# Performance work log

Hardware: AMD Instinct MI355X
Metric: run time of the kernel (lower is better)

The kernel has to match this reference:

```python
import jax, jax.numpy as jnp
import numpy as np
from jax import lax

BETA = 0.25  # args.beta

def setup_inputs() -> dict:
    key = jax.random.key(0)
    k1, k2 = jax.random.split(key)
    B, C, H, W = 32, 256, 32, 32
    K = 8192  # codebook_size; C == latent_dim
    z = jax.random.normal(k1, (B, C, H, W), dtype=jnp.float32)
    embedding = jax.random.normal(k2, (K, C), dtype=jnp.float32)
    return {"z": z, "embedding": embedding}

def reference(z, embedding):
    B, C, H, W = z.shape
    # rearrange 'b c h w -> b (h w) c'
    zf = z.reshape(B, C, H * W).transpose(0, 2, 1)  # [B, HW, C]
    # squared Euclidean distances (same argmin as torch.cdist): ||z||^2 - 2 z.e + ||e||^2
    d2 = (
        jnp.sum(zf * zf, axis=-1, keepdims=True)
        - 2.0 * jnp.einsum('bnc,kc->bnk', zf, embedding)
        + jnp.sum(embedding * embedding, axis=-1)
    )  # [B, HW, K]
    min_d = jnp.argmin(d2, axis=-1)  # [B, HW] int
    # faithful to original: .view((B, C, H, W)) is a raw reshape of [B, HW, C]
    z_q = embedding[min_d].reshape(B, C, H, W)
    commitment_loss = jnp.mean((lax.stop_gradient(z_q) - z) ** 2)
    codebook_loss = jnp.mean((lax.stop_gradient(z) - z_q) ** 2)
    loss = codebook_loss + BETA * commitment_loss
    # faithful to original straight-through variant: z - (z_q - z).detach()
    z_q_out = z - lax.stop_gradient(z_q - z)
    return z_q_out, min_d, loss
```

## Files before the change

kernel.cpp:

```cpp
#include <hip/hip_runtime.h>

#define CDIM    256
#define HWDIM   1024
#define KCB     8192
#define OUT_ZQ  8388608
#define OUT_MD  32768

__global__ void vq_init_kernel(float* p) {
    if (threadIdx.x == 0 && blockIdx.x == 0) p[0] = 0.0f;
}

__global__ __launch_bounds__(256) void vq_enorm_kernel(const float* __restrict__ emb,
                                                       float* __restrict__ enorm) {
    const int w    = threadIdx.x >> 6;
    const int lane = threadIdx.x & 63;
    const int k    = blockIdx.x * 4 + w;
    float4 v = *(const float4*)(emb + (size_t)k * CDIM + lane * 4);
    float s = v.x * v.x + v.y * v.y + v.z * v.z + v.w * v.w;
    #pragma unroll
    for (int off = 32; off > 0; off >>= 1) s += __shfl_down(s, off);
    if (lane == 0) enorm[k] = s;
}

__global__ __launch_bounds__(512) void vq_argmin_kernel(const float* __restrict__ z,
                                                        const float* __restrict__ emb,
                                                        const float* __restrict__ enorm,
                                                        float* __restrict__ mind_out) {
    __shared__ float zt[256][64];
    __shared__ float et[2][32][64];

    const int tid = threadIdx.x;
    const int tx  = tid & 15;
    const int ty  = tid >> 4;
    const int n0  = blockIdx.x * 64;
    const int b   = n0 >> 10;
    const int hw0 = n0 & 1023;
    const float* zb = z + (size_t)b * (CDIM * HWDIM) + hw0;

    for (int idx = tid; idx < 256 * 16; idx += 512) {
        const int c = idx >> 4, q4 = idx & 15;
        *(float4*)&zt[c][q4 * 4] = *(const float4*)(zb + (size_t)c * HWDIM + q4 * 4);
    }

    const int kk   = tid >> 3;
    const int c4   = tid & 7;
    const int ecol = kk ^ (c4 << 3);

    {
        float4 ev = *(const float4*)(emb + (size_t)kk * CDIM + c4 * 4);
        et[0][c4 * 4 + 0][ecol] = ev.x;
        et[0][c4 * 4 + 1][ecol] = ev.y;
        et[0][c4 * 4 + 2][ecol] = ev.z;
        et[0][c4 * 4 + 3][ecol] = ev.w;
    }
    __syncthreads();

    float bmin[2];
    int   bidx[2];
    #pragma unroll
    for (int i = 0; i < 2; ++i) { bmin[i] = 3.4e38f; bidx[i] = 0; }

    float acc[2][4];
    float4 en4;

    const int NCHUNK = (KCB / 64) * (CDIM / 32);
    int cur = 0;
    for (int t = 0; t < NCHUNK; ++t) {
        float4 nv;
        const bool hasnext = (t + 1) < NCHUNK;
        if (hasnext) {
            const int tn  = t + 1;
            const int nk0 = (tn >> 3) * 64;
            const int nc0 = (tn & 7) * 32;
            nv = *(const float4*)(emb + (size_t)(nk0 + kk) * CDIM + nc0 + c4 * 4);
        }
        if ((t & 7) == 0) {
            #pragma unroll
            for (int i = 0; i < 2; ++i)
                #pragma unroll
                for (int j = 0; j < 4; ++j) acc[i][j] = 0.0f;
            en4 = *(const float4*)(enorm + (t >> 3) * 64 + tx * 4);
        }
        const int c0 = (t & 7) * 32;

        #pragma unroll
        for (int ci = 0; ci < 32; ++ci) {
            float2 zf = *(const float2*)&zt[c0 + ci][ty * 2];
            float4 ef = *(const float4*)&et[cur][ci][(tx * 4) ^ ((ci >> 2) << 3)];
            const float* zp = reinterpret_cast<const float*>(&zf);
            const float* ep = reinterpret_cast<const float*>(&ef);
            #pragma unroll
            for (int i = 0; i < 2; ++i)
                #pragma unroll
                for (int j = 0; j < 4; ++j)
                    acc[i][j] += zp[i] * ep[j];
        }

        if (hasnext) {
            et[cur ^ 1][c4 * 4 + 0][ecol] = nv.x;
            et[cur ^ 1][c4 * 4 + 1][ecol] = nv.y;
            et[cur ^ 1][c4 * 4 + 2][ecol] = nv.z;
            et[cur ^ 1][c4 * 4 + 3][ecol] = nv.w;
        }

        if ((t & 7) == 7) {
            const int k0 = (t >> 3) * 64;
            const float* en = reinterpret_cast<const float*>(&en4);
            #pragma unroll
            for (int j = 0; j < 4; ++j) {
                const int kid = k0 + tx * 4 + j;
                #pragma unroll
                for (int i = 0; i < 2; ++i) {
                    const float s = en[j] - 2.0f * acc[i][j];
                    if (s < bmin[i]) { bmin[i] = s; bidx[i] = kid; }
                }
            }
        }
        __syncthreads();
        cur ^= 1;
    }

    float* redv = &zt[0][0];
    int*   redi = (int*)&zt[16][0];
    #pragma unroll
    for (int i = 0; i < 2; ++i) {
        const int q = ty * 2 + i;
        redv[q * 16 + tx] = bmin[i];
        redi[q * 16 + tx] = bidx[i];
    }
    __syncthreads();
    if (tid < 64) {
        const int q = tid;
        float bv = redv[q * 16 + 0];
        int   bi = redi[q * 16 + 0];
        #pragma unroll
        for (int t = 1; t < 16; ++t) {
            const float v = redv[q * 16 + t];
            const int  id = redi[q * 16 + t];
            if (v < bv || (v == bv && id < bi)) { bv = v; bi = id; }
        }
        mind_out[n0 + q] = (float)bi;
    }
}

__global__ __launch_bounds__(256) void vq_gather_kernel(const float* __restrict__ z,
                                                        const float* __restrict__ emb,
                                                        const float* __restrict__ mind,
                                                        float* __restrict__ out,
                                                        float* __restrict__ loss_accum) {
    const int tid = blockIdx.x * 256 + threadIdx.x;
    const int total4 = OUT_ZQ / 4;
    float lsum = 0.0f;
    for (int i4 = tid; i4 < total4; i4 += gridDim.x * 256) {
        const int idx = i4 * 4;
        const int b   = idx >> 18;
        const int f   = idx & 262143;
        const int nn  = f >> 8;
        const int cpr = f & 255;
        const int k   = (int)mind[b * 1024 + nn];
        float4 e4 = *(const float4*)(emb + (size_t)k * CDIM + cpr);
        float4 z4 = *(const float4*)(z + idx);
        float4 o;
        o.x = 2.0f * z4.x - e4.x;
        o.y = 2.0f * z4.y - e4.y;
        o.z = 2.0f * z4.z - e4.z;
        o.w = 2.0f * z4.w - e4.w;
        *(float4*)(out + idx) = o;
        const float dx = e4.x - z4.x, dy = e4.y - z4.y, dz = e4.z - z4.z, dw = e4.w - z4.w;
        lsum += dx * dx + dy * dy + dz * dz + dw * dw;
    }
    #pragma unroll
    for (int off = 32; off > 0; off >>= 1) lsum += __shfl_down(lsum, off);
    __shared__ float wsum[4];
    const int lane = threadIdx.x & 63, w = threadIdx.x >> 6;
    if (lane == 0) wsum[w] = lsum;
    __syncthreads();
    if (threadIdx.x == 0) atomicAdd(loss_accum, wsum[0] + wsum[1] + wsum[2] + wsum[3]);
}

__global__ void vq_final_kernel(float* lossp) {
    if (threadIdx.x == 0 && blockIdx.x == 0)
        lossp[0] = 1.25f * lossp[0] / 8388608.0f;
}

extern "C" void kernel_launch(void* const* d_in, const int* in_sizes, int n_in,
                              void* d_out, int out_size, void* d_ws, size_t ws_size,
                              hipStream_t stream) {
    const float* z   = (const float*)d_in[0];
    const float* emb = (const float*)d_in[1];
    float* out   = (float*)d_out;
    float* mind  = out + OUT_ZQ;
    float* lossp = out + OUT_ZQ + OUT_MD;
    float* enorm = out;

    vq_init_kernel<<<1, 64, 0, stream>>>(lossp);
    vq_enorm_kernel<<<2048, 256, 0, stream>>>(emb, enorm);
    vq_argmin_kernel<<<512, 512, 0, stream>>>(z, emb, enorm, mind);
    vq_gather_kernel<<<2048, 256, 0, stream>>>(z, emb, mind, out, lossp);
    vq_final_kernel<<<1, 64, 0, stream>>>(lossp);
}
```

Baseline: 2.358 ms.

## Compute distance GEMM with split-fp16 MFMA instead of scalar FP32 FMAs

The FP32 CUDA-core style distance tile loop is replaced by MFMA 16x16x32 fp16 instructions. Both z and the codebook are split into hi/lo fp16 parts so three products (hh, hl, lh) approximate the fp32 dot product. A new pre-kernel converts the codebook into swizzled hi/lo fp16 buffers held in scratch space in the output. The z operands stay resident in registers while codebook tiles are double-buffered through LDS, and the argmin reduction uses cross-lane shuffles. The split-fp16 scheme drops the lo*lo term and can lose accuracy, which risks changing argmin results on near-ties.

After: 1.915 ms. 18.8% less time.

```diff
diff --git a/kernel.cpp b/kernel.cpp
--- a/kernel.cpp
+++ b/kernel.cpp
@@ -5,6 +5,10 @@
 #define KCB     8192
 #define OUT_ZQ  8388608
 #define OUT_MD  32768
+#define KT      512
+
+typedef _Float16 f16x8 __attribute__((ext_vector_type(8)));
+typedef float    f32x4 __attribute__((ext_vector_type(4)));
 
 __global__ void vq_init_kernel(float* p) {
     if (threadIdx.x == 0 && blockIdx.x == 0) p[0] = 0.0f;
@@ -22,125 +26,163 @@
     if (lane == 0) enorm[k] = s;
 }
 
-__global__ __launch_bounds__(512) void vq_argmin_kernel(const float* __restrict__ z,
-                                                        const float* __restrict__ emb,
-                                                        const float* __restrict__ enorm,
-                                                        float* __restrict__ mind_out) {
-    __shared__ float zt[256][64];
-    __shared__ float et[2][32][64];
-
-    const int tid = threadIdx.x;
-    const int tx  = tid & 15;
-    const int ty  = tid >> 4;
-    const int n0  = blockIdx.x * 64;
-    const int b   = n0 >> 10;
-    const int hw0 = n0 & 1023;
-    const float* zb = z + (size_t)b * (CDIM * HWDIM) + hw0;
-
-    for (int idx = tid; idx < 256 * 16; idx += 512) {
-        const int c = idx >> 4, q4 = idx & 15;
-        *(float4*)&zt[c][q4 * 4] = *(const float4*)(zb + (size_t)c * HWDIM + q4 * 4);
-    }
-
-    const int kk   = tid >> 3;
-    const int c4   = tid & 7;
-    const int ecol = kk ^ (c4 << 3);
-
-    {
-        float4 ev = *(const float4*)(emb + (size_t)kk * CDIM + c4 * 4);
-        et[0][c4 * 4 + 0][ecol] = ev.x;
-        et[0][c4 * 4 + 1][ecol] = ev.y;
-        et[0][c4 * 4 + 2][ecol] = ev.z;
-        et[0][c4 * 4 + 3][ecol] = ev.w;
+__global__ __launch_bounds__(256) void vq_ecvt_kernel(const float* __restrict__ emb,
+                                                      _Float16* __restrict__ ehi,
+                                                      _Float16* __restrict__ elo) {
+    const int gid = blockIdx.x * 256 + threadIdx.x;
+    const int k = gid >> 5;
+    const int x = gid & 31;
+    const float* src = emb + (size_t)k * CDIM + x * 8;
+    float4 v0 = *(const float4*)(src);
+    float4 v1 = *(const float4*)(src + 4);
+    const float tmp[8] = {v0.x, v0.y, v0.z, v0.w, v1.x, v1.y, v1.z, v1.w};
+    f16x8 hi, lo;
+    #pragma unroll
+    for (int j = 0; j < 8; ++j) {
+        _Float16 h = (_Float16)tmp[j];
+        hi[j] = h;
+        lo[j] = (_Float16)(tmp[j] - (float)h);
+    }
+    const int xs = x ^ (k & 7);
+    *(f16x8*)(ehi + (size_t)k * CDIM + xs * 8) = hi;
+    *(f16x8*)(elo + (size_t)k * CDIM + xs * 8) = lo;
+}
+
+__global__ __launch_bounds__(128, 1) void vq_argmin_kernel(const float* __restrict__ z,
+                                                           const _Float16* __restrict__ ehi,
+                                                           const _Float16* __restrict__ elo,
+                                                           const float* __restrict__ enorm,
+                                                           float* __restrict__ mind_out) {
+    __shared__ _Float16 eb[2][2][16 * CDIM];
+
+    const int tid  = threadIdx.x;
+    const int lane = tid & 63;
+    const int wv   = tid >> 6;
+    const int l15  = lane & 15;
+    const int l4   = lane >> 4;
+
+    f16x8 a_hi[2][8], a_lo[2][8];
+    #pragma unroll
+    for (int qt = 0; qt < 2; ++qt) {
+        const int q0 = blockIdx.x * 64 + (wv * 2 + qt) * 16;
+        const int n  = q0 + l15;
+        const int b  = n >> 10;
+        const int hw = n & 1023;
+        const float* zb = z + (size_t)b * (CDIM * HWDIM) + hw;
+        #pragma unroll
+        for (int cc = 0; cc < 8; ++cc) {
+            #pragma unroll
+            for (int j = 0; j < 8; ++j) {
+                const int c = cc * 32 + l4 * 8 + j;
+                const float v = zb[(size_t)c * HWDIM];
+                const _Float16 h = (_Float16)v;
+                a_hi[qt][cc][j] = h;
+                a_lo[qt][cc][j] = (_Float16)(v - (float)h);
+            }
+        }
+    }
+
+    float4 greg[8];
+    #pragma unroll
+    for (int i = 0; i < 8; ++i) {
+        const int u = tid + i * 128;
+        const int h = u >> 9, kl = (u >> 5) & 15, x = u & 31;
+        const _Float16* g = (h ? elo : ehi) + (size_t)kl * CDIM + x * 8;
+        greg[i] = *(const float4*)g;
+    }
+    #pragma unroll
+    for (int i = 0; i < 8; ++i) {
+        const int u = tid + i * 128;
+        *(float4*)((_Float16*)eb + (size_t)u * 8) = greg[i];
+    }
+    #pragma unroll
+    for (int i = 0; i < 8; ++i) {
+        const int u = tid + i * 128;
+        const int h = u >> 9, kl = (u >> 5) & 15, x = u & 31;
+        const _Float16* g = (h ? elo : ehi) + (size_t)(16 + kl) * CDIM + x * 8;
+        greg[i] = *(const float4*)g;
     }
     __syncthreads();
 
-    float bmin[2];
-    int   bidx[2];
-    #pragma unroll
-    for (int i = 0; i < 2; ++i) { bmin[i] = 3.4e38f; bidx[i] = 0; }
-
-    float acc[2][4];
-    float4 en4;
-
-    const int NCHUNK = (KCB / 64) * (CDIM / 32);
-    int cur = 0;
-    for (int t = 0; t < NCHUNK; ++t) {
-        float4 nv;
-        const bool hasnext = (t + 1) < NCHUNK;
-        if (hasnext) {
-            const int tn  = t + 1;
-            const int nk0 = (tn >> 3) * 64;
-            const int nc0 = (tn & 7) * 32;
-            nv = *(const float4*)(emb + (size_t)(nk0 + kk) * CDIM + nc0 + c4 * 4);
-        }
-        if ((t & 7) == 0) {
-            #pragma unroll
-            for (int i = 0; i < 2; ++i)
-                #pragma unroll
-                for (int j = 0; j < 4; ++j) acc[i][j] = 0.0f;
-            en4 = *(const float4*)(enorm + (t >> 3) * 64 + tx * 4);
-        }
-        const int c0 = (t & 7) * 32;
-
-        #pragma unroll
-        for (int ci = 0; ci < 32; ++ci) {
-            float2 zf = *(const float2*)&zt[c0 + ci][ty * 2];
-            float4 ef = *(const float4*)&et[cur][ci][(tx * 4) ^ ((ci >> 2) << 3)];
-            const float* zp = reinterpret_cast<const float*>(&zf);
-            const float* ep = reinterpret_cast<const float*>(&ef);
-            #pragma unroll
-            for (int i = 0; i < 2; ++i)
-                #pragma unroll
-                for (int j = 0; j < 4; ++j)
-                    acc[i][j] += zp[i] * ep[j];
-        }
-
-        if (hasnext) {
-            et[cur ^ 1][c4 * 4 + 0][ecol] = nv.x;
-            et[cur ^ 1][c4 * 4 + 1][ecol] = nv.y;
-            et[cur ^ 1][c4 * 4 + 2][ecol] = nv.z;
-            et[cur ^ 1][c4 * 4 + 3][ecol] = nv.w;
-        }
-
-        if ((t & 7) == 7) {
-            const int k0 = (t >> 3) * 64;
-            const float* en = reinterpret_cast<const float*>(&en4);
-            #pragma unroll
-            for (int j = 0; j < 4; ++j) {
-                const int kid = k0 + tx * 4 + j;
-                #pragma unroll
-                for (int i = 0; i < 2; ++i) {
-                    const float s = en[j] - 2.0f * acc[i][j];
-                    if (s < bmin[i]) { bmin[i] = s; bidx[i] = kid; }
-                }
-            }
-        }
+    float bmin[2][4];
+    int   bidx[2][4];
+    #pragma unroll
+    for (int qt = 0; qt < 2; ++qt)
+        #pragma unroll
+        for (int r = 0; r < 4; ++r) { bmin[qt][r] = 3.4e38f; bidx[qt][r] = 0; }
+
+    const f32x4 vzero = {0.f, 0.f, 0.f, 0.f};
+
+    for (int t = 0; t < KT; ++t) {
+        const int cur = t & 1;
+        const int k0  = t * 16;
+        const float en = enorm[k0 + l15];
+
+        f32x4 acc_hh[2], acc_hl[2], acc_lh[2];
+        #pragma unroll
+        for (int qt = 0; qt < 2; ++qt) { acc_hh[qt] = vzero; acc_hl[qt] = vzero; acc_lh[qt] = vzero; }
+
+        const _Float16* ebh = &eb[cur][0][0];
+        const _Float16* ebl = &eb[cur][1][0];
+        #pragma unroll
+        for (int cc = 0; cc < 8; ++cc) {
+            const int xp = (cc * 4 + l4) ^ (l15 & 7);
+            const f16x8 bh = *(const f16x8*)(ebh + l15 * CDIM + xp * 8);
+            const f16x8 bl = *(const f16x8*)(ebl + l15 * CDIM + xp * 8);
+            #pragma unroll
+            for (int qt = 0; qt < 2; ++qt) {
+                acc_hh[qt] = __builtin_amdgcn_mfma_f32_16x16x32_f16(a_hi[qt][cc], bh, acc_hh[qt], 0, 0, 0);
+                acc_hl[qt] = __builtin_amdgcn_mfma_f32_16x16x32_f16(a_hi[qt][cc], bl, acc_hl[qt], 0, 0, 0);
+                acc_lh[qt] = __builtin_amdgcn_mfma_f32_16x16x32_f16(a_lo[qt][cc], bh, acc_lh[qt], 0, 0, 0);
+            }
+        }
+
+        if (t + 1 < KT) {
+            #pragma unroll
+            for (int i = 0; i < 8; ++i) {
+                const int u = tid + i * 128;
+                *(float4*)((_Float16*)eb + (size_t)(cur ^ 1) * 8192 + (size_t)u * 8) = greg[i];
+            }
+        }
+        if (t + 2 < KT) {
+            const int kb = (t + 2) * 16;
+            #pragma unroll
+            for (int i = 0; i < 8; ++i) {
+                const int u = tid + i * 128;
+                const int h = u >> 9, kl = (u >> 5) & 15, x = u & 31;
+                const _Float16* g = (h ? elo : ehi) + (size_t)(kb + kl) * CDIM + x * 8;
+                greg[i] = *(const float4*)g;
+            }
+        }
+
+        #pragma unroll
+        for (int qt = 0; qt < 2; ++qt)
+            #pragma unroll
+            for (int r = 0; r < 4; ++r) {
+                const float dot = acc_hh[qt][r] + acc_hl[qt][r] + acc_lh[qt][r];
+                const float s = en - 2.0f * dot;
+                if (s < bmin[qt][r]) { bmin[qt][r] = s; bidx[qt][r] = k0 + l15; }
+            }
         __syncthreads();
-        cur ^= 1;
-    }
-
-    float* redv = &zt[0][0];
-    int*   redi = (int*)&zt[16][0];
-    #pragma unroll
-    for (int i = 0; i < 2; ++i) {
-        const int q = ty * 2 + i;
-        redv[q * 16 + tx] = bmin[i];
-        redi[q * 16 + tx] = bidx[i];
-    }
-    __syncthreads();
-    if (tid < 64) {
-        const int q = tid;
-        float bv = redv[q * 16 + 0];
-        int   bi = redi[q * 16 + 0];
-        #pragma unroll
-        for (int t = 1; t < 16; ++t) {
-            const float v = redv[q * 16 + t];
-            const int  id = redi[q * 16 + t];
-            if (v < bv || (v == bv && id < bi)) { bv = v; bi = id; }
-        }
-        mind_out[n0 + q] = (float)bi;
-    }
+    }
+
+    #pragma unroll
+    for (int qt = 0; qt < 2; ++qt)
+        #pragma unroll
+        for (int r = 0; r < 4; ++r) {
+            float bv = bmin[qt][r];
+            int   bi = bidx[qt][r];
+            #pragma unroll
+            for (int m = 1; m < 16; m <<= 1) {
+                const float ov = __shfl_xor(bv, m, 64);
+                const int   oi = __shfl_xor(bi, m, 64);
+                if (ov < bv || (ov == bv && oi < bi)) { bv = ov; bi = oi; }
+            }
+            if (l15 == 0) {
+                const int q = blockIdx.x * 64 + (wv * 2 + qt) * 16 + l4 * 4 + r;
+                mind_out[q] = (float)bi;
+            }
+        }
 }
 
 __global__ __launch_bounds__(256) void vq_gather_kernel(const float* __restrict__ z,
@@ -191,11 +233,14 @@
     float* out   = (float*)d_out;
     float* mind  = out + OUT_ZQ;
     float* lossp = out + OUT_ZQ + OUT_MD;
-    float* enorm = out;
+    float*     enorm = out;
+    _Float16*  ehi   = (_Float16*)(out + 8192);
+    _Float16*  elo   = (_Float16*)(out + 8192 + 1048576);
 
     vq_init_kernel<<<1, 64, 0, stream>>>(lossp);
     vq_enorm_kernel<<<2048, 256, 0, stream>>>(emb, enorm);
-    vq_argmin_kernel<<<512, 512, 0, stream>>>(z, emb, enorm, mind);
+    vq_ecvt_kernel<<<1024, 256, 0, stream>>>(emb, ehi, elo);
+    vq_argmin_kernel<<<512, 128, 0, stream>>>(z, ehi, elo, enorm, mind);
     vq_gather_kernel<<<2048, 256, 0, stream>>>(z, emb, mind, out, lossp);
     vq_final_kernel<<<1, 64, 0, stream>>>(lossp);
 }
```
